# Performance work log

Measured on AMD Instinct MI355X. Metric: run time of the kernel, lower is better.

## Reference

```python
import jax, jax.numpy as jnp
import numpy as np

FEATURES_M = 1_000_000
HIDDEN = 64
LAYERS = [128, 64]
BATCH = 16384
N_FIELDS = 50


def setup_inputs() -> dict:
    key = jax.random.key(0)
    ks = jax.random.split(key, 12)
    inp = {
        "features": jax.random.randint(ks[0], (BATCH, N_FIELDS), 0, FEATURES_M, dtype=jnp.int32),
        "labels": jax.random.normal(ks[1], (BATCH, 1), dtype=jnp.float32),
        # learned parameters
        "emb_table": jax.random.normal(ks[2], (FEATURES_M, HIDDEN), dtype=jnp.float32) * 0.01,
        "bias_table": jax.random.normal(ks[3], (FEATURES_M, 1), dtype=jnp.float32) * 0.01,
        "w_bias": jax.random.normal(ks[4], (1, 1), dtype=jnp.float32),  # Dense(1, use_bias=False)
        "W1": jax.random.normal(ks[5], (HIDDEN, LAYERS[0]), dtype=jnp.float32) * (1.0 / np.sqrt(HIDDEN)),
        "b1": jnp.zeros((LAYERS[0],), dtype=jnp.float32),
        "W2": jax.random.normal(ks[6], (LAYERS[0], LAYERS[1]), dtype=jnp.float32) * (1.0 / np.sqrt(LAYERS[0])),
        "b2": jnp.zeros((LAYERS[1],), dtype=jnp.float32),
        "Wp": jax.random.normal(ks[7], (LAYERS[1], 1), dtype=jnp.float32) * (1.0 / np.sqrt(LAYERS[1])),
        "bp": jnp.zeros((1,), dtype=jnp.float32),
    }
    return inp


def reference(features, labels, emb_table, bias_table, w_bias, W1, b1, W2, b2, Wp, bp):
    # Embedding gather: [B, F, D]
    nonzero_emb = emb_table[features]
    # FM bi-interaction pooling: 0.5 * ((sum e)^2 - sum(e^2))  -> [B, D]
    summed = jnp.sum(nonzero_emb, axis=1)
    squared_sum = jnp.sum(jnp.square(nonzero_emb), axis=1)
    fm = 0.5 * (jnp.square(summed) - squared_sum)
    # Deep MLP stack (batch_norm off, dropout identity at eval keep_prob=1)
    h = jax.nn.relu(fm @ W1 + b1)
    h = jax.nn.relu(h @ W2 + b2)
    pred = h @ Wp + bp  # [B, 1]
    bilinear = jnp.sum(pred, axis=1, keepdims=True)  # [B, 1]
    # First-order feature bias: gather [B, F, 1] then sum over fields
    feature_bias = jnp.sum(bias_table[features], axis=1)  # [B, 1]
    # Global bias: Dense(1, no bias) applied to ones_like(labels)
    global_bias = jnp.ones_like(labels) @ w_bias  # [B, 1]
    return bilinear + feature_bias + global_bias
```

## Files before the change

### kernel.cpp

```cpp
#include <hip/hip_runtime.h>


#define NFIELDS 50
#define HIDDEN  64
#define L1N     128
#define L2N     64
#define RPW     8
#define WAVES   4
#define ROWS_PER_BLOCK (RPW * WAVES)

__global__ __launch_bounds__(256, 2) void neuralfm_kernel(
    const int*   __restrict__ features,
    const float* __restrict__ emb,
    const float* __restrict__ bias_t,
    const float* __restrict__ w_bias,
    const float* __restrict__ W1,
    const float* __restrict__ b1,
    const float* __restrict__ W2,
    const float* __restrict__ b2,
    const float* __restrict__ Wp,
    const float* __restrict__ bp,
    float*       __restrict__ out)
{
    __shared__ int   sIdx[WAVES][RPW * NFIELDS];
    __shared__ float sFm [WAVES][RPW * HIDDEN];
    __shared__ float sH1 [WAVES][RPW * L1N];

    const int tid  = threadIdx.x;
    const int wave = tid >> 6;
    const int lane = tid & 63;
    const int row0 = blockIdx.x * ROWS_PER_BLOCK + wave * RPW;

    const int idx_base = row0 * NFIELDS;
    #pragma unroll
    for (int t = lane; t < RPW * NFIELDS; t += 64)
        sIdx[wave][t] = features[idx_base + t];
    __syncthreads();

    float sum[RPW], sq[RPW];
    #pragma unroll
    for (int r = 0; r < RPW; ++r) { sum[r] = 0.f; sq[r] = 0.f; }

    for (int f = 0; f < NFIELDS; ++f) {
        #pragma unroll
        for (int r = 0; r < RPW; ++r) {
            const int   idx = sIdx[wave][r * NFIELDS + f];
            const float v   = emb[(size_t)idx * HIDDEN + lane];
            sum[r] += v;
            sq[r]  += v * v;
        }
    }
    #pragma unroll
    for (int r = 0; r < RPW; ++r)
        sFm[wave][r * HIDDEN + lane] = 0.5f * (sum[r] * sum[r] - sq[r]);
    __syncthreads();

    float h1a[RPW], h1b[RPW];
    #pragma unroll
    for (int r = 0; r < RPW; ++r) { h1a[r] = 0.f; h1b[r] = 0.f; }

    for (int d = 0; d < HIDDEN; ++d) {
        const float w0 = W1[d * L1N + lane];
        const float w1 = W1[d * L1N + 64 + lane];
        #pragma unroll
        for (int r = 0; r < RPW; ++r) {
            const float fv = sFm[wave][r * HIDDEN + d];
            h1a[r] += fv * w0;
            h1b[r] += fv * w1;
        }
    }
    const float bias1a = b1[lane];
    const float bias1b = b1[64 + lane];
    #pragma unroll
    for (int r = 0; r < RPW; ++r) {
        sH1[wave][r * L1N + lane]      = fmaxf(h1a[r] + bias1a, 0.f);
        sH1[wave][r * L1N + 64 + lane] = fmaxf(h1b[r] + bias1b, 0.f);
    }
    __syncthreads();

    float h2[RPW];
    #pragma unroll
    for (int r = 0; r < RPW; ++r) h2[r] = 0.f;

    for (int j = 0; j < L1N; ++j) {
        const float w = W2[j * L2N + lane];
        #pragma unroll
        for (int r = 0; r < RPW; ++r)
            h2[r] += sH1[wave][r * L1N + j] * w;
    }
    const float bias2 = b2[lane];
    const float wp    = Wp[lane];

    float tot[RPW];
    #pragma unroll
    for (int r = 0; r < RPW; ++r)
        tot[r] = fmaxf(h2[r] + bias2, 0.f) * wp;

    if (lane < NFIELDS) {
        #pragma unroll
        for (int r = 0; r < RPW; ++r)
            tot[r] += bias_t[sIdx[wave][r * NFIELDS + lane]];
    }

    #pragma unroll
    for (int r = 0; r < RPW; ++r) {
        float v = tot[r];
        #pragma unroll
        for (int off = 32; off > 0; off >>= 1)
            v += __shfl_xor(v, off, 64);
        tot[r] = v;
    }
    if (lane == 0) {
        const float c = bp[0] + w_bias[0];
        #pragma unroll
        for (int r = 0; r < RPW; ++r)
            out[row0 + r] = tot[r] + c;
    }
}

extern "C" void kernel_launch(void* const* d_in, const int* in_sizes, int n_in,
                              void* d_out, int out_size, void* d_ws, size_t ws_size,
                              hipStream_t stream) {
    const int*   features = (const int*)  d_in[0];
    const float* emb      = (const float*)d_in[2];
    const float* bias_t   = (const float*)d_in[3];
    const float* w_bias   = (const float*)d_in[4];
    const float* W1       = (const float*)d_in[5];
    const float* b1       = (const float*)d_in[6];
    const float* W2       = (const float*)d_in[7];
    const float* b2       = (const float*)d_in[8];
    const float* Wp       = (const float*)d_in[9];
    const float* bp       = (const float*)d_in[10];
    float*       out      = (float*)d_out;

    const int batch  = in_sizes[0] / NFIELDS;
    const int blocks = batch / ROWS_PER_BLOCK;

    neuralfm_kernel<<<blocks, 256, 0, stream>>>(
        features, emb, bias_t, w_bias, W1, b1, W2, b2, Wp, bp, out);
}
```

Baseline: 364.1 us.

## Gather embeddings with float4 per 16-lane subgroup, halve rows per wave

```diff
diff --git a/kernel.cpp b/kernel.cpp
--- a/kernel.cpp
+++ b/kernel.cpp
@@ -5,11 +5,11 @@
 #define HIDDEN  64
 #define L1N     128
 #define L2N     64
-#define RPW     8
+#define RPW     4
 #define WAVES   4
 #define ROWS_PER_BLOCK (RPW * WAVES)
 
-__global__ __launch_bounds__(256, 2) void neuralfm_kernel(
+__global__ __launch_bounds__(256, 4) void neuralfm_kernel(
     const int*   __restrict__ features,
     const float* __restrict__ emb,
     const float* __restrict__ bias_t,
@@ -22,13 +22,15 @@
     const float* __restrict__ bp,
     float*       __restrict__ out)
 {
-    __shared__ int   sIdx[WAVES][RPW * NFIELDS];
-    __shared__ float sFm [WAVES][RPW * HIDDEN];
-    __shared__ float sH1 [WAVES][RPW * L1N];
+    __shared__ int    sIdx[WAVES][RPW * NFIELDS];
+    __shared__ float4 sFm4[WAVES][RPW * HIDDEN / 4];
+    __shared__ float  sH1 [WAVES][RPW * L1N];
 
     const int tid  = threadIdx.x;
     const int wave = tid >> 6;
     const int lane = tid & 63;
+    const int sub  = lane >> 4;
+    const int le   = lane & 15;
     const int row0 = blockIdx.x * ROWS_PER_BLOCK + wave * RPW;
 
     const int idx_base = row0 * NFIELDS;
@@ -37,36 +39,50 @@
         sIdx[wave][t] = features[idx_base + t];
     __syncthreads();
 
-    float sum[RPW], sq[RPW];
+    float biasacc[RPW];
     #pragma unroll
-    for (int r = 0; r < RPW; ++r) { sum[r] = 0.f; sq[r] = 0.f; }
+    for (int r = 0; r < RPW; ++r) biasacc[r] = 0.f;
+    if (lane < NFIELDS) {
+        #pragma unroll
+        for (int r = 0; r < RPW; ++r)
+            biasacc[r] = bias_t[sIdx[wave][r * NFIELDS + lane]];
+    }
 
+    const float4* __restrict__ emb4 = (const float4*)emb;
+    float sx = 0.f, sy = 0.f, sz = 0.f, sw = 0.f;
+    float qx = 0.f, qy = 0.f, qz = 0.f, qw = 0.f;
+    const int* myIdx = &sIdx[wave][sub * NFIELDS];
+    #pragma unroll
     for (int f = 0; f < NFIELDS; ++f) {
-        #pragma unroll
-        for (int r = 0; r < RPW; ++r) {
-            const int   idx = sIdx[wave][r * NFIELDS + f];
-            const float v   = emb[(size_t)idx * HIDDEN + lane];
-            sum[r] += v;
-            sq[r]  += v * v;
-        }
+        const int    idx = myIdx[f];
+        const float4 v   = emb4[(size_t)idx * (HIDDEN / 4) + le];
+        sx += v.x; sy += v.y; sz += v.z; sw += v.w;
+        qx += v.x * v.x; qy += v.y * v.y; qz += v.z * v.z; qw += v.w * v.w;
     }
-    #pragma unroll
-    for (int r = 0; r < RPW; ++r)
-        sFm[wave][r * HIDDEN + lane] = 0.5f * (sum[r] * sum[r] - sq[r]);
+    float4 fm;
+    fm.x = 0.5f * (sx * sx - qx);
+    fm.y = 0.5f * (sy * sy - qy);
+    fm.z = 0.5f * (sz * sz - qz);
+    fm.w = 0.5f * (sw * sw - qw);
+    sFm4[wave][sub * (HIDDEN / 4) + le] = fm;
     __syncthreads();
 
     float h1a[RPW], h1b[RPW];
     #pragma unroll
     for (int r = 0; r < RPW; ++r) { h1a[r] = 0.f; h1b[r] = 0.f; }
 
-    for (int d = 0; d < HIDDEN; ++d) {
-        const float w0 = W1[d * L1N + lane];
-        const float w1 = W1[d * L1N + 64 + lane];
+    for (int dq = 0; dq < HIDDEN / 4; ++dq) {
+        float w0[4], w1[4];
+        #pragma unroll
+        for (int c = 0; c < 4; ++c) {
+            w0[c] = W1[(4 * dq + c) * L1N + lane];
+            w1[c] = W1[(4 * dq + c) * L1N + 64 + lane];
+        }
         #pragma unroll
         for (int r = 0; r < RPW; ++r) {
-            const float fv = sFm[wave][r * HIDDEN + d];
-            h1a[r] += fv * w0;
-            h1b[r] += fv * w1;
+            const float4 fv = sFm4[wave][r * (HIDDEN / 4) + dq];
+            h1a[r] += fv.x * w0[0] + fv.y * w0[1] + fv.z * w0[2] + fv.w * w0[3];
+            h1b[r] += fv.x * w1[0] + fv.y * w1[1] + fv.z * w1[2] + fv.w * w1[3];
         }
     }
     const float bias1a = b1[lane];
@@ -78,15 +94,21 @@
     }
     __syncthreads();
 
+    const float4* sH14 = (const float4*)&sH1[wave][0];
     float h2[RPW];
     #pragma unroll
     for (int r = 0; r < RPW; ++r) h2[r] = 0.f;
 
-    for (int j = 0; j < L1N; ++j) {
-        const float w = W2[j * L2N + lane];
+    for (int jq = 0; jq < L1N / 4; ++jq) {
+        float w[4];
         #pragma unroll
-        for (int r = 0; r < RPW; ++r)
-            h2[r] += sH1[wave][r * L1N + j] * w;
+        for (int c = 0; c < 4; ++c)
+            w[c] = W2[(4 * jq + c) * L2N + lane];
+        #pragma unroll
+        for (int r = 0; r < RPW; ++r) {
+            const float4 hv = sH14[r * (L1N / 4) + jq];
+            h2[r] += hv.x * w[0] + hv.y * w[1] + hv.z * w[2] + hv.w * w[3];
+        }
     }
     const float bias2 = b2[lane];
     const float wp    = Wp[lane];
@@ -94,13 +116,7 @@
     float tot[RPW];
     #pragma unroll
     for (int r = 0; r < RPW; ++r)
-        tot[r] = fmaxf(h2[r] + bias2, 0.f) * wp;
-
-    if (lane < NFIELDS) {
-        #pragma unroll
-        for (int r = 0; r < RPW; ++r)
-            tot[r] += bias_t[sIdx[wave][r * NFIELDS + lane]];
-    }
+        tot[r] = fmaxf(h2[r] + bias2, 0.f) * wp + biasacc[r];
 
     #pragma unroll
     for (int r = 0; r < RPW; ++r) {
```

Result: faster. 354.5 us (-2.7%).
